# Kernel optimization log

Measured on AMD Instinct MI355X. Metric: run time of the kernel, lower is better.

The kernel has to match this reference:

```python
import jax, jax.numpy as jnp
import numpy as np

VOXEL_SIZE = np.array([0.1, 0.05, 0.05], dtype=np.float32)  # (z, y, x)
COOR_OFFSET = np.array([-3.0, -40.0, 0.0], dtype=np.float32)  # (z, y, x)
KERNEL, PAD = 3, 1


def setup_inputs() -> dict:
    key = jax.random.key(0)
    ks = jax.random.split(key, 12)
    B, N, Cv, Cr, H, W = 4, 40000, 16, 32, 376, 1248
    # sparse voxel coords: (batch, z, y, x) on the KITTI 40x1600x1408 grid
    bidx = jax.random.randint(ks[0], (N, 1), 0, B)
    z = jax.random.randint(ks[1], (N, 1), 0, 40)
    y = jax.random.randint(ks[2], (N, 1), 0, 1600)
    x = jax.random.randint(ks[3], (N, 1), 0, 1408)
    voxel_coords = jnp.concatenate([bidx, z, y, x], axis=1).astype(jnp.int32)
    voxel_features = jax.random.normal(ks[4], (N, Cv), jnp.float32)
    rgb_features = jax.random.normal(ks[5], (B, Cr, H, W), jnp.float32)
    # KITTI-like calibration: P2 intrinsics, Trv2c lidar->cam, rect ~ I
    fu, fv, cu, cv = 720.0, 720.0, W / 2.0, H / 2.0
    P2_base = jnp.array([[fu, 0.0, cu, 44.9], [0.0, fv, cv, 0.1], [0.0, 0.0, 1.0, 0.003]], jnp.float32)
    P2 = jnp.tile(P2_base[None], (B, 1, 1)) + 0.01 * jax.random.normal(ks[6], (B, 3, 4), jnp.float32)
    T_base = jnp.array([[0.0, -1.0, 0.0, 0.0], [0.0, 0.0, -1.0, -0.08], [1.0, 0.0, 0.0, -0.27], [0.0, 0.0, 0.0, 1.0]], jnp.float32)
    Trv2c = jnp.tile(T_base[None], (B, 1, 1)) + 0.001 * jax.random.normal(ks[7], (B, 4, 4), jnp.float32)
    rect = jnp.tile(jnp.eye(4, dtype=jnp.float32)[None], (B, 1, 1)) + 0.001 * jax.random.normal(ks[8], (B, 4, 4), jnp.float32)
    rgb_coor_refine = 0.5 * jax.random.normal(ks[9], (B, 2), jnp.float32)
    dummy_batch_list = jnp.arange(B, dtype=jnp.int32)
    return {"voxel_features": voxel_features, "rgb_features": rgb_features, "P2": P2,
            "Trv2c": Trv2c, "rect": rect, "rgb_coor_refine": rgb_coor_refine,
            "voxel_coords": voxel_coords, "dummy_batch_list": dummy_batch_list}


def _fuse(voxel_features, rgb_features, P2, Trv2c, rect, rgb_coor_refine, voxel_coords, dummy_batch_list):
    B, Cr, H, W = rgb_features.shape
    N, Cv = voxel_features.shape
    # per-batch gather as in the torch forward's dummy lists
    rgb = rgb_features[dummy_batch_list]            # [B, Cr, H, W]
    P2d = P2[dummy_batch_list]                      # [B, 3, 4]
    Md = jnp.einsum('bij,bjk->bik', rect[dummy_batch_list], Trv2c[dummy_batch_list])  # [B,4,4]
    prd = rgb_coor_refine[dummy_batch_list]         # [B, 2]
    # simple sparse-tensor expansion: dilate each voxel to its kernel^3 neighborhood
    r = jnp.arange(-PAD, KERNEL - PAD)
    off = jnp.stack(jnp.meshgrid(r, r, r, indexing='ij'), axis=-1).reshape(-1, 3)  # [K3,3]
    K3 = off.shape[0]
    zyx = (voxel_coords[:, None, 1:] + off[None]).reshape(-1, 3)  # [M,3]
    b = jnp.broadcast_to(voxel_coords[:, 0:1], (N, K3)).reshape(-1)  # [M]
    M = zyx.shape[0]
    # voxel center in lidar frame: zyx -> xyz
    ctr_zyx = (zyx.astype(jnp.float32) + 0.5) * jnp.asarray(VOXEL_SIZE) + jnp.asarray(COOR_OFFSET)
    xyz1 = jnp.concatenate([ctr_zyx[:, ::-1], jnp.ones((M, 1), jnp.float32)], axis=1)  # [M,4]
    cam = jnp.einsum('mij,mj->mi', Md[b], xyz1)      # [M,4] camera frame
    img = jnp.einsum('mij,mj->mi', P2d[b], cam)      # [M,3] homogeneous pixels
    depth = img[:, 2]
    d = jnp.maximum(depth, 1e-3)
    u = img[:, 0] / d + prd[b, 0]
    v = img[:, 1] / d + prd[b, 1]
    valid = (depth > 1e-3) & (u >= 0) & (u <= W - 1) & (v >= 0) & (v <= H - 1)
    uc = jnp.clip(u, 0.0, W - 1.0)
    vc = jnp.clip(v, 0.0, H - 1.0)
    x0 = jnp.floor(uc).astype(jnp.int32); y0 = jnp.floor(vc).astype(jnp.int32)
    x1 = jnp.minimum(x0 + 1, W - 1);      y1 = jnp.minimum(y0 + 1, H - 1)
    wx = (uc - x0.astype(jnp.float32))[:, None]
    wy = (vc - y0.astype(jnp.float32))[:, None]
    f00 = rgb[b, :, y0, x0]; f10 = rgb[b, :, y0, x1]
    f01 = rgb[b, :, y1, x0]; f11 = rgb[b, :, y1, x1]
    samp = (f00 * (1 - wx) * (1 - wy) + f10 * wx * (1 - wy)
            + f01 * (1 - wx) * wy + f11 * wx * wy)
    samp = samp * valid[:, None].astype(samp.dtype)  # zero features outside image
    vf = jnp.broadcast_to(voxel_features[:, None, :], (N, K3, Cv)).reshape(M, Cv)
    return jnp.concatenate([vf, samp], axis=1)       # [M, Cv + Cr]


def reference(voxel_features, rgb_features, P2, Trv2c, rect, rgb_coor_refine, voxel_coords, dummy_batch_list):
    return _fuse(voxel_features, rgb_features, P2, Trv2c, rect, rgb_coor_refine, voxel_coords, dummy_batch_list)
```

## Files before the change

kernel.cpp:

```cpp
#include <hip/hip_runtime.h>

namespace {
constexpr int IMG_H = 376;
constexpr int IMG_W = 1248;
constexpr int CV = 16;
constexpr int CR = 32;
constexpr int CO = CV + CR;
constexpr int K3 = 27;
constexpr int BLOCK = 256;
constexpr int LDS_STRIDE = CO + 1;
}

__global__ void prep_kernel(const float* __restrict__ P2,
                            const float* __restrict__ Trv2c,
                            const float* __restrict__ rect,
                            const float* __restrict__ prd,
                            const int* __restrict__ dummy,
                            float* __restrict__ mats, int B) {
    int b = threadIdx.x;
    if (b >= B) return;
    int s = dummy[b];
    float* o = mats + b * 32;
    const float* R = rect + s * 16;
    const float* T = Trv2c + s * 16;
    for (int i = 0; i < 4; ++i) {
        for (int j = 0; j < 4; ++j) {
            float acc = R[i * 4 + 0] * T[0 * 4 + j];
            acc += R[i * 4 + 1] * T[1 * 4 + j];
            acc += R[i * 4 + 2] * T[2 * 4 + j];
            acc += R[i * 4 + 3] * T[3 * 4 + j];
            o[i * 4 + j] = acc;
        }
    }
    for (int i = 0; i < 12; ++i) o[16 + i] = P2[s * 12 + i];
    o[28] = prd[s * 2 + 0];
    o[29] = prd[s * 2 + 1];
}

__global__ __launch_bounds__(BLOCK) void fuse_kernel(
        const float* __restrict__ vfeat,
        const float* __restrict__ rgb,
        const float* __restrict__ mats,
        const int* __restrict__ vcoords,
        float* __restrict__ out,
        int N) {
    const int M = N * K3;
    __shared__ float lds[BLOCK][LDS_STRIDE];

    const int t = threadIdx.x;
    const int m = blockIdx.x * BLOCK + t;

    if (m < M) {
        int n = m / K3;
        int kk = m - n * K3;
        int4 vc = ((const int4*)vcoords)[n];
        int b = vc.x;
        int dz = kk / 9;
        int rem = kk - dz * 9;
        int dy = rem / 3;
        int dx = rem - dy * 3;

        float fz = ((float)(vc.y + dz - 1) + 0.5f) * 0.1f - 3.0f;
        float fy = ((float)(vc.z + dy - 1) + 0.5f) * 0.05f - 40.0f;
        float fx = ((float)(vc.w + dx - 1) + 0.5f) * 0.05f;

        const float* Mb = mats + b * 32;
        float cam0 = Mb[0]  * fx + Mb[1]  * fy + Mb[2]  * fz + Mb[3];
        float cam1 = Mb[4]  * fx + Mb[5]  * fy + Mb[6]  * fz + Mb[7];
        float cam2 = Mb[8]  * fx + Mb[9]  * fy + Mb[10] * fz + Mb[11];
        float cam3 = Mb[12] * fx + Mb[13] * fy + Mb[14] * fz + Mb[15];

        float img0 = Mb[16] * cam0 + Mb[17] * cam1 + Mb[18] * cam2 + Mb[19] * cam3;
        float img1 = Mb[20] * cam0 + Mb[21] * cam1 + Mb[22] * cam2 + Mb[23] * cam3;
        float img2 = Mb[24] * cam0 + Mb[25] * cam1 + Mb[26] * cam2 + Mb[27] * cam3;

        float depth = img2;
        float d = fmaxf(depth, 0.001f);
        float u = img0 / d + Mb[28];
        float v = img1 / d + Mb[29];

        bool valid = (depth > 0.001f) && (u >= 0.0f) && (u <= (float)(IMG_W - 1))
                     && (v >= 0.0f) && (v <= (float)(IMG_H - 1));

        const float* vp = vfeat + (size_t)n * CV;
        #pragma unroll
        for (int c = 0; c < CV; ++c) lds[t][c] = vp[c];

        if (valid) {
            float uc = fminf(fmaxf(u, 0.0f), (float)(IMG_W - 1));
            float vcl = fminf(fmaxf(v, 0.0f), (float)(IMG_H - 1));
            int x0 = (int)floorf(uc);
            int y0 = (int)floorf(vcl);
            int x1 = min(x0 + 1, IMG_W - 1);
            int y1 = min(y0 + 1, IMG_H - 1);
            float wx = uc - (float)x0;
            float wy = vcl - (float)y0;
            float w00 = (1.0f - wx) * (1.0f - wy);
            float w10 = wx * (1.0f - wy);
            float w01 = (1.0f - wx) * wy;
            float w11 = wx * wy;
            const float* base = rgb + (size_t)b * CR * IMG_H * IMG_W;
            int o00 = y0 * IMG_W + x0;
            int o10 = y0 * IMG_W + x1;
            int o01 = y1 * IMG_W + x0;
            int o11 = y1 * IMG_W + x1;
            #pragma unroll
            for (int c = 0; c < CR; ++c) {
                const float* p = base + (size_t)c * (IMG_H * IMG_W);
                float s = p[o00] * w00 + p[o10] * w10 + p[o01] * w01 + p[o11] * w11;
                lds[t][CV + c] = s;
            }
        } else {
            #pragma unroll
            for (int c = 0; c < CR; ++c) lds[t][CV + c] = 0.0f;
        }
    }

    __syncthreads();

    size_t blockBase = (size_t)blockIdx.x * BLOCK * CO;
    size_t total = (size_t)M * CO;
    #pragma unroll 4
    for (int i = 0; i < CO; ++i) {
        int f = i * BLOCK + t;
        int r = f / CO;
        int c = f - r * CO;
        size_t g = blockBase + (size_t)f;
        if (g < total) out[g] = lds[r][c];
    }
}

extern "C" void kernel_launch(void* const* d_in, const int* in_sizes, int n_in,
                              void* d_out, int out_size, void* d_ws, size_t ws_size,
                              hipStream_t stream) {
    const float* vfeat  = (const float*)d_in[0];
    const float* rgb    = (const float*)d_in[1];
    const float* P2     = (const float*)d_in[2];
    const float* Trv2c  = (const float*)d_in[3];
    const float* rect   = (const float*)d_in[4];
    const float* prd    = (const float*)d_in[5];
    const int* vcoords  = (const int*)d_in[6];
    const int* dummy    = (const int*)d_in[7];
    float* out = (float*)d_out;

    int B = in_sizes[7];
    int N = in_sizes[6] / 4;
    float* mats = (float*)d_ws;

    prep_kernel<<<1, 64, 0, stream>>>(P2, Trv2c, rect, prd, dummy, mats, B);

    int M = N * K3;
    int blocks = (M + BLOCK - 1) / BLOCK;
    fuse_kernel<<<blocks, BLOCK, 0, stream>>>(vfeat, rgb, mats, vcoords, out, N);
}
```

Before: 142.0 us.

## Stage output per-wave through small LDS and store with float4

Keeps each thread's 48 output values in registers, then transposes per wave through a 16-row LDS tile in four rounds. This replaces the block-wide barrier with wave barriers and lets the output be written as coalesced float4 stores. Voxel features are also loaded as float4. In exchange it uses more registers for the s[48] array and adds serialized rounds of LDS traffic per wave.

```diff
diff --git a/kernel.cpp b/kernel.cpp
--- a/kernel.cpp
+++ b/kernel.cpp
@@ -3,12 +3,13 @@
 namespace {
 constexpr int IMG_H = 376;
 constexpr int IMG_W = 1248;
+constexpr int HW = IMG_H * IMG_W;
 constexpr int CV = 16;
 constexpr int CR = 32;
 constexpr int CO = CV + CR;
 constexpr int K3 = 27;
 constexpr int BLOCK = 256;
-constexpr int LDS_STRIDE = CO + 1;
+constexpr int LDSPAD = CO + 1;
 }
 
 __global__ void prep_kernel(const float* __restrict__ P2,
@@ -45,12 +46,20 @@
         float* __restrict__ out,
         int N) {
     const int M = N * K3;
-    __shared__ float lds[BLOCK][LDS_STRIDE];
+    __shared__ float lds[4][16][LDSPAD];
 
     const int t = threadIdx.x;
-    const int m = blockIdx.x * BLOCK + t;
+    const int wave = t >> 6;
+    const int lane = t & 63;
+    const int waveBase = blockIdx.x * BLOCK + wave * 64;
+    const int m = waveBase + lane;
+    const bool inR = (m < M);
 
-    if (m < M) {
+    float s[CO];
+    #pragma unroll
+    for (int c = 0; c < CO; ++c) s[c] = 0.0f;
+
+    if (inR) {
         int n = m / K3;
         int kk = m - n * K3;
         int4 vc = ((const int4*)vcoords)[n];
@@ -82,9 +91,12 @@
         bool valid = (depth > 0.001f) && (u >= 0.0f) && (u <= (float)(IMG_W - 1))
                      && (v >= 0.0f) && (v <= (float)(IMG_H - 1));
 
-        const float* vp = vfeat + (size_t)n * CV;
-        #pragma unroll
-        for (int c = 0; c < CV; ++c) lds[t][c] = vp[c];
+        const float4* vp4 = (const float4*)(vfeat + (size_t)n * CV);
+        float4 vf0 = vp4[0], vf1 = vp4[1], vf2 = vp4[2], vf3 = vp4[3];
+        s[0] = vf0.x;  s[1] = vf0.y;  s[2]  = vf0.z;  s[3]  = vf0.w;
+        s[4] = vf1.x;  s[5] = vf1.y;  s[6]  = vf1.z;  s[7]  = vf1.w;
+        s[8] = vf2.x;  s[9] = vf2.y;  s[10] = vf2.z;  s[11] = vf2.w;
+        s[12] = vf3.x; s[13] = vf3.y; s[14] = vf3.z;  s[15] = vf3.w;
 
         if (valid) {
             float uc = fminf(fmaxf(u, 0.0f), (float)(IMG_W - 1));
@@ -99,34 +111,46 @@
             float w10 = wx * (1.0f - wy);
             float w01 = (1.0f - wx) * wy;
             float w11 = wx * wy;
-            const float* base = rgb + (size_t)b * CR * IMG_H * IMG_W;
+            const float* base = rgb + (size_t)b * CR * HW;
             int o00 = y0 * IMG_W + x0;
             int o10 = y0 * IMG_W + x1;
             int o01 = y1 * IMG_W + x0;
             int o11 = y1 * IMG_W + x1;
             #pragma unroll
             for (int c = 0; c < CR; ++c) {
-                const float* p = base + (size_t)c * (IMG_H * IMG_W);
-                float s = p[o00] * w00 + p[o10] * w10 + p[o01] * w01 + p[o11] * w11;
-                lds[t][CV + c] = s;
+                const float* p = base + (size_t)c * HW;
+                s[CV + c] = p[o00] * w00 + p[o10] * w10
+                          + p[o01] * w01 + p[o11] * w11;
             }
-        } else {
-            #pragma unroll
-            for (int c = 0; c < CR; ++c) lds[t][CV + c] = 0.0f;
         }
     }
 
-    __syncthreads();
-
-    size_t blockBase = (size_t)blockIdx.x * BLOCK * CO;
-    size_t total = (size_t)M * CO;
-    #pragma unroll 4
-    for (int i = 0; i < CO; ++i) {
-        int f = i * BLOCK + t;
-        int r = f / CO;
-        int c = f - r * CO;
-        size_t g = blockBase + (size_t)f;
-        if (g < total) out[g] = lds[r][c];
+    const size_t total = (size_t)M * CO;
+    #pragma unroll 1
+    for (int j = 0; j < 4; ++j) {
+        __builtin_amdgcn_wave_barrier();
+        if ((lane >> 4) == j && inR) {
+            int r = lane & 15;
+            #pragma unroll
+            for (int c = 0; c < CO; ++c) lds[wave][r][c] = s[c];
+        }
+        __builtin_amdgcn_wave_barrier();
+        size_t chunkBase = ((size_t)waveBase + (size_t)j * 16) * CO;
+        #pragma unroll
+        for (int i = 0; i < 3; ++i) {
+            int g = i * 64 + lane;
+            int row = g / 12;
+            int c4 = (g - row * 12) * 4;
+            float4 val = make_float4(lds[wave][row][c4 + 0],
+                                     lds[wave][row][c4 + 1],
+                                     lds[wave][row][c4 + 2],
+                                     lds[wave][row][c4 + 3]);
+            size_t idx = chunkBase + (size_t)g * 4;
+            if (idx < total) {
+                *(float4*)(out + idx) = val;
+            }
+        }
+        __builtin_amdgcn_wave_barrier();
     }
 }
 
```

Result: no change. 141.6 us (-0.3%).
